# Kernel tuning notes

Hardware: AMD Instinct MI355X
Metric: run time of the kernel (lower is better)

## Reference

```python
import jax, jax.numpy as jnp
import numpy as np

N = 8192
D_IN = 128
D_OUT = 128


def setup_inputs() -> dict:
    key = jax.random.key(0)
    k1, k2, k3 = jax.random.split(key, 3)
    node_features = jax.random.normal(k1, (N, D_IN), dtype=jnp.float32)
    adj_matrix = jax.random.uniform(k2, (N, N), dtype=jnp.float32)
    # Xavier-uniform weight, zero bias (as in reset_parameters)
    limit = float(np.sqrt(6.0 / (D_IN + D_OUT)))
    weight = jax.random.uniform(k3, (D_IN, D_OUT), dtype=jnp.float32,
                                minval=-limit, maxval=limit)
    bias = jnp.zeros((D_OUT,), dtype=jnp.float32)
    return {"node_features": node_features, "adj_matrix": adj_matrix,
            "weight": weight, "bias": bias}


def reference(node_features, adj_matrix, weight, bias):
    n = adj_matrix.shape[0]
    # A_hat = A + I
    a_hat = adj_matrix + jnp.eye(n, dtype=adj_matrix.dtype)
    d_hat = jnp.sum(a_hat, axis=1)  # [N]
    # pow(d, -0.5) with inf (d==0) masked to 0
    d_inv_sqrt = jnp.where(d_hat > 0, jax.lax.rsqrt(d_hat), 0.0)
    # diag(d) @ A_hat @ diag(d) == row/col broadcast scaling (same math)
    adj_normalized = d_inv_sqrt[:, None] * a_hat * d_inv_sqrt[None, :]
    support = node_features @ weight  # [N, D_OUT]
    out = adj_normalized @ support + bias
    return out
```

## Files before the change

kernel.cpp:

```cpp
#include <hip/hip_runtime.h>

#define NN 8192
#define DD 128

typedef short s16x4 __attribute__((ext_vector_type(4)));
typedef short s16x8 __attribute__((ext_vector_type(8)));
typedef float f32x4 __attribute__((ext_vector_type(4)));

__device__ __forceinline__ unsigned short f2bf(float f) {
  unsigned int u = __float_as_uint(f);
  u += 0x7fffu + ((u >> 16) & 1u);
  return (unsigned short)(u >> 16);
}
__device__ __forceinline__ float bf2f(unsigned short h) {
  return __uint_as_float(((unsigned int)h) << 16);
}

__global__ __launch_bounds__(256) void k_rowsum(const float* __restrict__ A,
                                                float* __restrict__ dinv) {
  const int row = blockIdx.x;
  const float4* Ar = (const float4*)(A + (size_t)row * NN);
  const int t = threadIdx.x;
  float s = 0.f;
#pragma unroll
  for (int i = 0; i < 8; ++i) {
    float4 v = Ar[t + 256 * i];
    s += (v.x + v.y) + (v.z + v.w);
  }
#pragma unroll
  for (int off = 32; off > 0; off >>= 1) s += __shfl_down(s, off, 64);
  __shared__ float red[4];
  if ((t & 63) == 0) red[t >> 6] = s;
  __syncthreads();
  if (t == 0) {
    float d = 1.0f + ((red[0] + red[1]) + (red[2] + red[3]));
    dinv[row] = d > 0.f ? rsqrtf(d) : 0.f;
  }
}

__global__ __launch_bounds__(256) void k_support(const float* __restrict__ X,
                                                 const float* __restrict__ W,
                                                 const float* __restrict__ dinv,
                                                 unsigned short* __restrict__ tT) {
  __shared__ __align__(16) unsigned short Wt[128][136];
  __shared__ __align__(16) unsigned short Xs[32][136];
  const int t = threadIdx.x;
  const int j0 = blockIdx.x * 32;

  const float4* W4 = (const float4*)W;
#pragma unroll
  for (int s = 0; s < 16; ++s) {
    int c = t + 256 * s;
    int k = c >> 5, n4 = c & 31;
    float4 wv = W4[c];
    Wt[n4 * 4 + 0][k] = f2bf(wv.x);
    Wt[n4 * 4 + 1][k] = f2bf(wv.y);
    Wt[n4 * 4 + 2][k] = f2bf(wv.z);
    Wt[n4 * 4 + 3][k] = f2bf(wv.w);
  }
  const float4* X4 = (const float4*)(X + (size_t)j0 * DD);
#pragma unroll
  for (int s = 0; s < 4; ++s) {
    int c = t + 256 * s;
    int j = c >> 5, q = c & 31;
    float4 xv = X4[c];
    s16x4 p;
    p[0] = (short)f2bf(xv.x); p[1] = (short)f2bf(xv.y);
    p[2] = (short)f2bf(xv.z); p[3] = (short)f2bf(xv.w);
    *(s16x4*)&Xs[j][q * 4] = p;
  }
  __syncthreads();

  const int w = t >> 6, L = t & 63, lrow = L & 15, quad = L >> 4;
  f32x4 acc[2][2] = {};
#pragma unroll
  for (int ks = 0; ks < 4; ++ks) {
    const int k = ks * 32;
    s16x8 fa[2], fb[2];
#pragma unroll
    for (int nt = 0; nt < 2; ++nt)
      fa[nt] = *(const s16x8*)&Wt[w * 32 + nt * 16 + lrow][k + quad * 8];
#pragma unroll
    for (int jt = 0; jt < 2; ++jt)
      fb[jt] = *(const s16x8*)&Xs[jt * 16 + lrow][k + quad * 8];
#pragma unroll
    for (int nt = 0; nt < 2; ++nt)
#pragma unroll
      for (int jt = 0; jt < 2; ++jt)
        acc[nt][jt] = __builtin_amdgcn_mfma_f32_16x16x32_bf16(fa[nt], fb[jt], acc[nt][jt], 0, 0, 0);
  }

#pragma unroll
  for (int jt = 0; jt < 2; ++jt) {
    const int j = j0 + jt * 16 + lrow;
    const float dv = dinv[j];
#pragma unroll
    for (int nt = 0; nt < 2; ++nt) {
#pragma unroll
      for (int r = 0; r < 4; ++r) {
        const int n = w * 32 + nt * 16 + quad * 4 + r;
        tT[(size_t)n * NN + j] = f2bf(dv * acc[nt][jt][r]);
      }
    }
  }
}

__global__ __launch_bounds__(256) void k_gemm(const float* __restrict__ A,
                                              const unsigned short* __restrict__ tT,
                                              const float* __restrict__ dinv,
                                              const float* __restrict__ bias,
                                              float* __restrict__ out) {
  __shared__ __align__(16) unsigned short Ash[2][32][72];
  __shared__ __align__(16) unsigned short Bsh[2][128][72];
  const int t = threadIdx.x;
  const int bm = blockIdx.x;
  const float* Abase = A + (size_t)bm * 32 * NN;
  const int w = t >> 6, L = t & 63, lrow = L & 15, quad = L >> 4;

  const int ar = t >> 4;
  const int akc = t & 15;
  const int bn = t >> 3;
  const int bkc = t & 7;

  float4 a0, a1;
  uint4 b0, b1, b2, b3;

  auto load_tile = [&](int k0) {
    const float* ab = Abase + k0;
    a0 = *(const float4*)(ab + (size_t)ar * NN + akc * 4);
    a1 = *(const float4*)(ab + (size_t)(ar + 16) * NN + akc * 4);
    const unsigned short* tb = tT + k0 + bkc * 8;
    b0 = *(const uint4*)(tb + (size_t)(bn +  0) * NN);
    b1 = *(const uint4*)(tb + (size_t)(bn + 32) * NN);
    b2 = *(const uint4*)(tb + (size_t)(bn + 64) * NN);
    b3 = *(const uint4*)(tb + (size_t)(bn + 96) * NN);
  };
  auto store_tile = [&](int buf) {
    s16x4 p;
    p[0]=(short)f2bf(a0.x); p[1]=(short)f2bf(a0.y); p[2]=(short)f2bf(a0.z); p[3]=(short)f2bf(a0.w);
    *(s16x4*)&Ash[buf][ar][akc * 4] = p;
    p[0]=(short)f2bf(a1.x); p[1]=(short)f2bf(a1.y); p[2]=(short)f2bf(a1.z); p[3]=(short)f2bf(a1.w);
    *(s16x4*)&Ash[buf][ar + 16][akc * 4] = p;
    *(uint4*)&Bsh[buf][bn +  0][bkc * 8] = b0;
    *(uint4*)&Bsh[buf][bn + 32][bkc * 8] = b1;
    *(uint4*)&Bsh[buf][bn + 64][bkc * 8] = b2;
    *(uint4*)&Bsh[buf][bn + 96][bkc * 8] = b3;
  };

  f32x4 acc[2][2] = {};
  load_tile(0);
  store_tile(0);
  __syncthreads();

  for (int it = 0; it < 128; ++it) {
    const int cur = it & 1;
    if (it < 127) load_tile((it + 1) * 64);
#pragma unroll
    for (int s = 0; s < 2; ++s) {
      s16x8 fa0 = *(const s16x8*)&Ash[cur][lrow][s * 32 + quad * 8];
      s16x8 fa1 = *(const s16x8*)&Ash[cur][16 + lrow][s * 32 + quad * 8];
      s16x8 fb0 = *(const s16x8*)&Bsh[cur][w * 32 + lrow][s * 32 + quad * 8];
      s16x8 fb1 = *(const s16x8*)&Bsh[cur][w * 32 + 16 + lrow][s * 32 + quad * 8];
      acc[0][0] = __builtin_amdgcn_mfma_f32_16x16x32_bf16(fa0, fb0, acc[0][0], 0, 0, 0);
      acc[0][1] = __builtin_amdgcn_mfma_f32_16x16x32_bf16(fa0, fb1, acc[0][1], 0, 0, 0);
      acc[1][0] = __builtin_amdgcn_mfma_f32_16x16x32_bf16(fa1, fb0, acc[1][0], 0, 0, 0);
      acc[1][1] = __builtin_amdgcn_mfma_f32_16x16x32_bf16(fa1, fb1, acc[1][1], 0, 0, 0);
    }
    if (it < 127) store_tile(cur ^ 1);
    __syncthreads();
  }

#pragma unroll
  for (int mt = 0; mt < 2; ++mt) {
#pragma unroll
    for (int r = 0; r < 4; ++r) {
      const int i = bm * 32 + mt * 16 + quad * 4 + r;
      const float dv = dinv[i];
#pragma unroll
      for (int nt = 0; nt < 2; ++nt) {
        const int n = w * 32 + nt * 16 + lrow;
        const float diag = bf2f(tT[(size_t)n * NN + i]);
        out[(size_t)i * DD + n] = dv * (acc[mt][nt][r] + diag) + bias[n];
      }
    }
  }
}

extern "C" void kernel_launch(void* const* d_in, const int* in_sizes, int n_in,
                              void* d_out, int out_size, void* d_ws, size_t ws_size,
                              hipStream_t stream) {
  const float* X    = (const float*)d_in[0];
  const float* A    = (const float*)d_in[1];
  const float* W    = (const float*)d_in[2];
  const float* bias = (const float*)d_in[3];
  float* out = (float*)d_out;

  float* dinv = (float*)d_ws;
  unsigned short* tT = (unsigned short*)((char*)d_ws + 32768);

  hipLaunchKernelGGL(k_rowsum,  dim3(8192), dim3(256), 0, stream, A, dinv);
  hipLaunchKernelGGL(k_support, dim3(256),  dim3(256), 0, stream, X, W, dinv, tT);
  hipLaunchKernelGGL(k_gemm,    dim3(256),  dim3(256), 0, stream, A, tT, dinv, bias, out);
}
```

Before: 475.7 us.

## Pre-convert A to bf16, split-K GEMM with async LDS loads and reduce pass

```diff
diff --git a/kernel.cpp b/kernel.cpp
--- a/kernel.cpp
+++ b/kernel.cpp
@@ -6,26 +6,34 @@
 typedef short s16x4 __attribute__((ext_vector_type(4)));
 typedef short s16x8 __attribute__((ext_vector_type(8)));
 typedef float f32x4 __attribute__((ext_vector_type(4)));
-
-__device__ __forceinline__ unsigned short f2bf(float f) {
+typedef unsigned short u16;
+typedef const void __attribute__((address_space(1))) gvoid;
+typedef void __attribute__((address_space(3))) lvoid;
+
+__device__ __forceinline__ u16 f2bf(float f) {
   unsigned int u = __float_as_uint(f);
   u += 0x7fffu + ((u >> 16) & 1u);
-  return (unsigned short)(u >> 16);
-}
-__device__ __forceinline__ float bf2f(unsigned short h) {
+  return (u16)(u >> 16);
+}
+__device__ __forceinline__ float bf2f(u16 h) {
   return __uint_as_float(((unsigned int)h) << 16);
 }
 
-__global__ __launch_bounds__(256) void k_rowsum(const float* __restrict__ A,
-                                                float* __restrict__ dinv) {
+__global__ __launch_bounds__(256) void k_prep(const float* __restrict__ A,
+                                              float* __restrict__ dinv,
+                                              u16* __restrict__ Abf) {
   const int row = blockIdx.x;
   const float4* Ar = (const float4*)(A + (size_t)row * NN);
+  ushort4* Br = (ushort4*)(Abf + (size_t)row * NN);
   const int t = threadIdx.x;
   float s = 0.f;
 #pragma unroll
   for (int i = 0; i < 8; ++i) {
     float4 v = Ar[t + 256 * i];
     s += (v.x + v.y) + (v.z + v.w);
+    ushort4 b;
+    b.x = f2bf(v.x); b.y = f2bf(v.y); b.z = f2bf(v.z); b.w = f2bf(v.w);
+    Br[t + 256 * i] = b;
   }
 #pragma unroll
   for (int off = 32; off > 0; off >>= 1) s += __shfl_down(s, off, 64);
@@ -41,9 +49,9 @@
 __global__ __launch_bounds__(256) void k_support(const float* __restrict__ X,
                                                  const float* __restrict__ W,
                                                  const float* __restrict__ dinv,
-                                                 unsigned short* __restrict__ tT) {
-  __shared__ __align__(16) unsigned short Wt[128][136];
-  __shared__ __align__(16) unsigned short Xs[32][136];
+                                                 u16* __restrict__ tT) {
+  __shared__ __align__(16) u16 Wt[128][136];
+  __shared__ __align__(16) u16 Xs[32][136];
   const int t = threadIdx.x;
   const int j0 = blockIdx.x * 32;
 
@@ -105,85 +113,95 @@
   }
 }
 
-__global__ __launch_bounds__(256) void k_gemm(const float* __restrict__ A,
-                                              const unsigned short* __restrict__ tT,
-                                              const float* __restrict__ dinv,
-                                              const float* __restrict__ bias,
-                                              float* __restrict__ out) {
-  __shared__ __align__(16) unsigned short Ash[2][32][72];
-  __shared__ __align__(16) unsigned short Bsh[2][128][72];
+#define TILE_BYTES 20480
+__global__ __launch_bounds__(256) void k_gemm(const u16* __restrict__ Abf,
+                                              const u16* __restrict__ tT,
+                                              float* __restrict__ part) {
+  __shared__ __align__(16) unsigned char sh[2][TILE_BYTES];
   const int t = threadIdx.x;
-  const int bm = blockIdx.x;
-  const float* Abase = A + (size_t)bm * 32 * NN;
+  const int bm = blockIdx.x >> 1;
+  const int kh = blockIdx.x & 1;
+  const int kbase = kh * (NN / 2);
   const int w = t >> 6, L = t & 63, lrow = L & 15, quad = L >> 4;
-
-  const int ar = t >> 4;
-  const int akc = t & 15;
-  const int bn = t >> 3;
-  const int bkc = t & 7;
-
-  float4 a0, a1;
-  uint4 b0, b1, b2, b3;
-
-  auto load_tile = [&](int k0) {
-    const float* ab = Abase + k0;
-    a0 = *(const float4*)(ab + (size_t)ar * NN + akc * 4);
-    a1 = *(const float4*)(ab + (size_t)(ar + 16) * NN + akc * 4);
-    const unsigned short* tb = tT + k0 + bkc * 8;
-    b0 = *(const uint4*)(tb + (size_t)(bn +  0) * NN);
-    b1 = *(const uint4*)(tb + (size_t)(bn + 32) * NN);
-    b2 = *(const uint4*)(tb + (size_t)(bn + 64) * NN);
-    b3 = *(const uint4*)(tb + (size_t)(bn + 96) * NN);
+  const size_t row0 = (size_t)bm * 32;
+
+  auto prefetch = [&](int buf, int k0) {
+#pragma unroll
+    for (int j = 0; j < 5; ++j) {
+      const int g = w * 5 + j;
+      const int o = g * 1024 + L * 16;
+      const u16* src;
+      if (g < 4) {
+        const int r = o >> 7, c = (o >> 4) & 7;
+        src = Abf + (row0 + r) * NN + (k0 + ((c ^ (r & 7)) << 3));
+      } else {
+        const int o2 = o - 4096;
+        const int r = o2 >> 7, c = (o2 >> 4) & 7;
+        src = tT + (size_t)r * NN + (k0 + ((c ^ (r & 7)) << 3));
+      }
+      __builtin_amdgcn_global_load_lds((gvoid*)src,
+                                       (lvoid*)&sh[buf][g * 1024], 16, 0, 0);
+    }
   };
-  auto store_tile = [&](int buf) {
-    s16x4 p;
-    p[0]=(short)f2bf(a0.x); p[1]=(short)f2bf(a0.y); p[2]=(short)f2bf(a0.z); p[3]=(short)f2bf(a0.w);
-    *(s16x4*)&Ash[buf][ar][akc * 4] = p;
-    p[0]=(short)f2bf(a1.x); p[1]=(short)f2bf(a1.y); p[2]=(short)f2bf(a1.z); p[3]=(short)f2bf(a1.w);
-    *(s16x4*)&Ash[buf][ar + 16][akc * 4] = p;
-    *(uint4*)&Bsh[buf][bn +  0][bkc * 8] = b0;
-    *(uint4*)&Bsh[buf][bn + 32][bkc * 8] = b1;
-    *(uint4*)&Bsh[buf][bn + 64][bkc * 8] = b2;
-    *(uint4*)&Bsh[buf][bn + 96][bkc * 8] = b3;
-  };
 
   f32x4 acc[2][2] = {};
-  load_tile(0);
-  store_tile(0);
+  prefetch(0, kbase);
   __syncthreads();
 
-  for (int it = 0; it < 128; ++it) {
+  for (int it = 0; it < 64; ++it) {
     const int cur = it & 1;
-    if (it < 127) load_tile((it + 1) * 64);
+    if (it < 63) prefetch(cur ^ 1, kbase + (it + 1) * 64);
+    const unsigned char* Ab = &sh[cur][0];
+    const unsigned char* Bb = &sh[cur][4096];
 #pragma unroll
     for (int s = 0; s < 2; ++s) {
-      s16x8 fa0 = *(const s16x8*)&Ash[cur][lrow][s * 32 + quad * 8];
-      s16x8 fa1 = *(const s16x8*)&Ash[cur][16 + lrow][s * 32 + quad * 8];
-      s16x8 fb0 = *(const s16x8*)&Bsh[cur][w * 32 + lrow][s * 32 + quad * 8];
-      s16x8 fb1 = *(const s16x8*)&Bsh[cur][w * 32 + 16 + lrow][s * 32 + quad * 8];
+      const int cx = (((s * 4) | quad) ^ (lrow & 7)) << 4;
+      s16x8 fa0 = *(const s16x8*)(Ab + lrow * 128 + cx);
+      s16x8 fa1 = *(const s16x8*)(Ab + (16 + lrow) * 128 + cx);
+      s16x8 fb0 = *(const s16x8*)(Bb + (w * 32 + lrow) * 128 + cx);
+      s16x8 fb1 = *(const s16x8*)(Bb + (w * 32 + 16 + lrow) * 128 + cx);
       acc[0][0] = __builtin_amdgcn_mfma_f32_16x16x32_bf16(fa0, fb0, acc[0][0], 0, 0, 0);
       acc[0][1] = __builtin_amdgcn_mfma_f32_16x16x32_bf16(fa0, fb1, acc[0][1], 0, 0, 0);
       acc[1][0] = __builtin_amdgcn_mfma_f32_16x16x32_bf16(fa1, fb0, acc[1][0], 0, 0, 0);
       acc[1][1] = __builtin_amdgcn_mfma_f32_16x16x32_bf16(fa1, fb1, acc[1][1], 0, 0, 0);
     }
-    if (it < 127) store_tile(cur ^ 1);
     __syncthreads();
   }
 
+  float* pbase = part + (size_t)kh * NN * DD;
 #pragma unroll
   for (int mt = 0; mt < 2; ++mt) {
 #pragma unroll
     for (int r = 0; r < 4; ++r) {
-      const int i = bm * 32 + mt * 16 + quad * 4 + r;
-      const float dv = dinv[i];
+      const int i = (int)row0 + mt * 16 + quad * 4 + r;
 #pragma unroll
       for (int nt = 0; nt < 2; ++nt) {
         const int n = w * 32 + nt * 16 + lrow;
-        const float diag = bf2f(tT[(size_t)n * NN + i]);
-        out[(size_t)i * DD + n] = dv * (acc[mt][nt][r] + diag) + bias[n];
+        pbase[(size_t)i * DD + n] = acc[mt][nt][r];
       }
     }
   }
+}
+
+__global__ __launch_bounds__(256) void k_reduce(const float* __restrict__ part,
+                                                const u16* __restrict__ tT,
+                                                const float* __restrict__ dinv,
+                                                const float* __restrict__ bias,
+                                                float* __restrict__ out) {
+  const int gid = blockIdx.x * 256 + threadIdx.x;
+  const int i = gid >> 5;
+  const int c = gid & 31;
+  const float4 p0 = ((const float4*)part)[(size_t)i * 32 + c];
+  const float4 p1 = ((const float4*)(part + (size_t)NN * DD))[(size_t)i * 32 + c];
+  const float4 bb = ((const float4*)bias)[c];
+  const float dv = dinv[i];
+  const int n = c * 4;
+  float4 o;
+  o.x = dv * (p0.x + p1.x + bf2f(tT[(size_t)(n + 0) * NN + i])) + bb.x;
+  o.y = dv * (p0.y + p1.y + bf2f(tT[(size_t)(n + 1) * NN + i])) + bb.y;
+  o.z = dv * (p0.z + p1.z + bf2f(tT[(size_t)(n + 2) * NN + i])) + bb.z;
+  o.w = dv * (p0.w + p1.w + bf2f(tT[(size_t)(n + 3) * NN + i])) + bb.w;
+  ((float4*)out)[(size_t)i * 32 + c] = o;
 }
 
 extern "C" void kernel_launch(void* const* d_in, const int* in_sizes, int n_in,
@@ -196,9 +214,12 @@
   float* out = (float*)d_out;
 
   float* dinv = (float*)d_ws;
-  unsigned short* tT = (unsigned short*)((char*)d_ws + 32768);
-
-  hipLaunchKernelGGL(k_rowsum,  dim3(8192), dim3(256), 0, stream, A, dinv);
+  u16*   tT   = (u16*)((char*)d_ws + 32768);
+  float* part = (float*)((char*)d_ws + 32768 + 2097152);
+  u16*   Abf  = (u16*)((char*)d_ws + 32768 + 2097152 + 8388608);
+
+  hipLaunchKernelGGL(k_prep,    dim3(8192), dim3(256), 0, stream, A, dinv, Abf);
   hipLaunchKernelGGL(k_support, dim3(256),  dim3(256), 0, stream, X, W, dinv, tT);
-  hipLaunchKernelGGL(k_gemm,    dim3(256),  dim3(256), 0, stream, A, tT, dinv, bias, out);
-}
+  hipLaunchKernelGGL(k_gemm,    dim3(512),  dim3(256), 0, stream, Abf, tT, part);
+  hipLaunchKernelGGL(k_reduce,  dim3(1024), dim3(256), 0, stream, part, tT, dinv, bias, out);
+}
```

Measured after the change: 456.6 us. -4.0%, faster.
